# Performance work log

Hardware: AMD Instinct MI355X
Metric: run time of the kernel (lower is better)

## Reference

```python
import jax, jax.numpy as jnp
import numpy as np

B, Hd, Wd, C, NH, WS = 8, 128, 128, 192, 6, 8
HDIM = int(C * 2.0)   # FFN hidden = 384
RED = C // 8          # AIM channel-gate reduction = 24


def setup_inputs() -> dict:
    key = jax.random.key(0)
    ks = jax.random.split(key, 12)
    s = 0.02
    return {
        "x": jax.random.normal(ks[0], (B, Hd * Wd, C), jnp.float32),
        "H": Hd,
        "W": Wd,
        "n1_w": jnp.ones((C,), jnp.float32),
        "n1_b": jnp.zeros((C,), jnp.float32),
        "qkv_w": jax.random.normal(ks[1], (C, 3 * C), jnp.float32) * s,
        "proj_w": jax.random.normal(ks[2], (C, C), jnp.float32) * s,
        "proj_b": jnp.zeros((C,), jnp.float32),
        "attn_bias": jax.random.normal(ks[3], (NH, WS * WS, WS * WS), jnp.float32) * s,
        "conv_w": jax.random.normal(ks[4], (C, 1, 3, 3), jnp.float32) * s,
        "cg_w1": jax.random.normal(ks[5], (RED, C), jnp.float32) * s,
        "cg_w2": jax.random.normal(ks[6], (C, RED), jnp.float32) * s,
        "n2_w": jnp.ones((C,), jnp.float32),
        "n2_b": jnp.zeros((C,), jnp.float32),
        "fc1_w": jax.random.normal(ks[7], (C, HDIM), jnp.float32) * s,
        "smix_w": jax.random.normal(ks[8], (HDIM, 1, 3, 3), jnp.float32) * s,
        "fc2_w": jax.random.normal(ks[9], (HDIM, C), jnp.float32) * s,
    }


def _ln(x, w, b):
    m = x.mean(-1, keepdims=True)
    v = ((x - m) ** 2).mean(-1, keepdims=True)
    return (x - m) * jax.lax.rsqrt(v + 1e-5) * w + b


def _dwconv(x, w, H, W):
    # x: [B, L, Cx] -> depthwise 3x3 'same' conv -> [B, L, Cx]
    Bx, L, Cx = x.shape
    xi = x.transpose(0, 2, 1).reshape(Bx, Cx, H, W)
    y = jax.lax.conv_general_dilated(
        xi, w, (1, 1), 'SAME', feature_group_count=Cx,
        dimension_numbers=('NCHW', 'OIHW', 'NCHW'))
    return y.reshape(Bx, Cx, L).transpose(0, 2, 1)


def _window_attn(x, H, W, qkv_w, proj_w, proj_b, bias):
    Bx, L, Cx = x.shape
    nHw, nWw = H // WS, W // WS  # H, W are multiples of WS here (no padding needed)
    hd = Cx // NH
    # [B, L, C] -> [B*nH*nW, ws*ws, C]
    xw = (x.reshape(Bx, nHw, WS, nWw, WS, Cx)
           .transpose(0, 1, 3, 2, 4, 5)
           .reshape(Bx * nHw * nWw, WS * WS, Cx))
    qkv = (xw @ qkv_w).reshape(-1, WS * WS, 3, NH, hd).transpose(2, 0, 3, 1, 4)
    q, k, v = qkv[0], qkv[1], qkv[2]          # [Bw, nh, N, hd]
    logits = (q * hd ** -0.5) @ k.transpose(0, 1, 3, 2) + bias[None]
    attn = jax.nn.softmax(logits, axis=-1)
    out = (attn @ v).transpose(0, 2, 1, 3).reshape(-1, WS * WS, Cx)
    out = out @ proj_w + proj_b
    # windows -> [B, L, C]
    return (out.reshape(Bx, nHw, nWw, WS, WS, Cx)
               .transpose(0, 1, 3, 2, 4, 5)
               .reshape(Bx, L, Cx))


def reference(x, H, W, n1_w, n1_b, qkv_w, proj_w, proj_b, attn_bias,
              conv_w, cg_w1, cg_w2, n2_w, n2_b, fc1_w, smix_w, fc2_w):
    n1 = _ln(x, n1_w, n1_b)
    attn_feat = _window_attn(n1, H, W, qkv_w, proj_w, proj_b, attn_bias)
    conv_feat = jax.nn.gelu(_dwconv(n1, conv_w, H, W), approximate=False)
    # AIM: channel_modulates_spatial (btype == 'spatial')
    pooled = conv_feat.mean(axis=1)                                   # [B, C]
    cm = jax.nn.sigmoid(jax.nn.gelu(pooled @ cg_w1.T, approximate=False) @ cg_w2.T)
    x = x + attn_feat * cm[:, None, :] + conv_feat                    # residual (DropPath=id)
    # FFN with depthwise spatial mixing
    n2 = _ln(x, n2_w, n2_b)
    h = jax.nn.gelu(n2 @ fc1_w, approximate=False)                    # [B, L, HDIM]
    h = _dwconv(h, smix_w, H, W)
    return x + h @ fc2_w
```

## Files before the change

kernel.cpp:

```cpp
#include <hip/hip_runtime.h>
#include <hip/hip_bf16.h>
#include <math.h>

#define BATCH 8
#define CCH 192
#define LTOK 16384
#define BL 131072LL
#define NWIN 2048
#define NHEADS 6

typedef __hip_bfloat16 bf16;
typedef __bf16 bfr;
typedef bfr bf16x8 __attribute__((ext_vector_type(8)));
typedef float f32x4 __attribute__((ext_vector_type(4)));
typedef unsigned short u16x8 __attribute__((ext_vector_type(8)));
typedef unsigned short u16x4 __attribute__((ext_vector_type(4)));
typedef unsigned int u32x2 __attribute__((ext_vector_type(2)));

#define FX     0
#define FN1W   1
#define FN1B   2
#define FQKVW  3
#define FPROJW 4
#define FPROJB 5
#define FBIAS  6
#define FCONVW 7
#define FCG1   8
#define FCG2   9
#define FN2W   10
#define FN2B   11
#define FFC1   12
#define FSMIX  13
#define FFC2   14

struct InPtrs { const void* p[15]; int n[15]; };

__device__ __forceinline__ float ldin(const void* p, long long i, int f32) {
    return f32 ? ((const float*)p)[i]
               : __bfloat162float(((const bf16*)p)[i]);
}

__device__ __forceinline__ float bfcvt(unsigned short u) {
    return __uint_as_float((unsigned)u << 16);
}

__device__ __forceinline__ f32x4 ld4f(const void* p, long long i, int f32) {
    if (f32) return *(const f32x4*)((const float*)p + i);
    u16x4 v = *(const u16x4*)((const bf16*)p + i);
    f32x4 r;
    r[0] = bfcvt(v[0]); r[1] = bfcvt(v[1]); r[2] = bfcvt(v[2]); r[3] = bfcvt(v[3]);
    return r;
}
__device__ __forceinline__ f32x4 ld4b(const bf16* p, long long i) {
    u16x4 v = *(const u16x4*)(p + i);
    f32x4 r;
    r[0] = bfcvt(v[0]); r[1] = bfcvt(v[1]); r[2] = bfcvt(v[2]); r[3] = bfcvt(v[3]);
    return r;
}
__device__ __forceinline__ void st4b(bf16* p, long long i, f32x4 v) {
    union { bf16 h; unsigned short u; } cv;
    u16x4 o;
    cv.h = __float2bfloat16(v[0]); o[0] = cv.u;
    cv.h = __float2bfloat16(v[1]); o[1] = cv.u;
    cv.h = __float2bfloat16(v[2]); o[2] = cv.u;
    cv.h = __float2bfloat16(v[3]); o[3] = cv.u;
    *(u16x4*)(p + i) = o;
}

__device__ __forceinline__ unsigned pk2bf(float a, float b) {
    union { bf16 h; unsigned short u; } ca, cb;
    ca.h = __float2bfloat16(a);
    cb.h = __float2bfloat16(b);
    return (unsigned)ca.u | ((unsigned)cb.u << 16);
}

__device__ __forceinline__ float gelu_f(float v) {
    return 0.5f * v * (1.0f + erff(v * 0.70710678118654752f));
}

__device__ int local_probe(const void* p_, int n) {
    __shared__ int sh0, sh1, sh2;
    if (threadIdx.x == 0) { sh0 = 0; sh1 = 0; sh2 = 0; }
    __syncthreads();
    const bf16* p = (const bf16*)p_;
    int m = n < 2048 ? n : 2048;
    bool insane = false, evennz = false, oddnz = false;
    for (int i = threadIdx.x; i < m; i += 256) {
        float v = __bfloat162float(p[i]);
        if (!(fabsf(v) <= 1e9f)) insane = true;
        if (v != 0.0f) { if (i & 1) oddnz = true; else evennz = true; }
    }
    if (insane) sh0 = 1;
    if (evennz) sh1 = 1;
    if (oddnz)  sh2 = 1;
    __syncthreads();
    return (sh0 || (!sh1 && sh2)) ? 1 : 0;
}

__global__ __launch_bounds__(256)
void prep_k(InPtrs ip, int* __restrict__ flags,
            bf16* __restrict__ qkv_wT, bf16* __restrict__ proj_wT,
            bf16* __restrict__ fc1_wT, bf16* __restrict__ fc2_wT,
            float* __restrict__ convwT, float* __restrict__ smixwT,
            float* __restrict__ pooled) {
    int blk = blockIdx.x;
    if (blk < 15) {
        int f = local_probe(ip.p[blk], ip.n[blk]);
        if (threadIdx.x == 0) flags[blk] = f;
        return;
    }
    blk -= 15;
    if (blk < 432) {
        int f = local_probe(ip.p[FQKVW], ip.n[FQKVW]);
        int idx = blk * 256 + threadIdx.x;
        int k = idx / 576, n = idx - k * 576;
        qkv_wT[(long long)n * 192 + k] = __float2bfloat16(ldin(ip.p[FQKVW], idx, f));
        return;
    }
    blk -= 432;
    if (blk < 144) {
        int f = local_probe(ip.p[FPROJW], ip.n[FPROJW]);
        int idx = blk * 256 + threadIdx.x;
        int k = idx / 192, n = idx - k * 192;
        proj_wT[(long long)n * 192 + k] = __float2bfloat16(ldin(ip.p[FPROJW], idx, f));
        return;
    }
    blk -= 144;
    if (blk < 288) {
        int f = local_probe(ip.p[FFC1], ip.n[FFC1]);
        int idx = blk * 256 + threadIdx.x;
        int k = idx / 384, n = idx - k * 384;
        fc1_wT[(long long)n * 192 + k] = __float2bfloat16(ldin(ip.p[FFC1], idx, f));
        return;
    }
    blk -= 288;
    if (blk < 288) {
        int f = local_probe(ip.p[FFC2], ip.n[FFC2]);
        int idx = blk * 256 + threadIdx.x;
        int k = idx / 192, n = idx - k * 192;
        fc2_wT[(long long)n * 384 + k] = __float2bfloat16(ldin(ip.p[FFC2], idx, f));
        return;
    }
    blk -= 288;
    if (blk < 7) {
        int f = local_probe(ip.p[FCONVW], ip.n[FCONVW]);
        int idx = blk * 256 + threadIdx.x;
        if (idx < 192 * 9) {
            int c = idx / 9, t = idx - c * 9;
            convwT[t * 192 + c] = ldin(ip.p[FCONVW], idx, f);
        }
        return;
    }
    blk -= 7;
    if (blk < 14) {
        int f = local_probe(ip.p[FSMIX], ip.n[FSMIX]);
        int idx = blk * 256 + threadIdx.x;
        if (idx < 384 * 9) {
            int c = idx / 9, t = idx - c * 9;
            smixwT[t * 384 + c] = ldin(ip.p[FSMIX], idx, f);
        }
        return;
    }
    blk -= 14;
    {
        int idx = blk * 256 + threadIdx.x;
        if (idx < BATCH * CCH) pooled[idx] = 0.f;
    }
}

__global__ __launch_bounds__(256)
void ln_kernel(const void* __restrict__ x, const void* __restrict__ w,
               const void* __restrict__ b, bf16* __restrict__ out,
               const int* flags) {
    int fx = flags[FX], fw = flags[FN1W], fb = flags[FN1B];
    int wv = threadIdx.x >> 6, lane = threadIdx.x & 63;
    int gw = lane >> 4, l16 = lane & 15;
    long long t = (long long)blockIdx.x * 16 + wv * 4 + gw;
    long long base = t * CCH;
    f32x4 v[3];
#pragma unroll
    for (int k = 0; k < 3; ++k)
        v[k] = ld4f(x, base + l16 * 4 + 64 * k, fx);
    float s = 0.f;
#pragma unroll
    for (int k = 0; k < 3; ++k) s += v[k][0] + v[k][1] + v[k][2] + v[k][3];
    s += __shfl_xor(s, 1); s += __shfl_xor(s, 2);
    s += __shfl_xor(s, 4); s += __shfl_xor(s, 8);
    float mean = s * (1.0f / 192.0f);
    float vs = 0.f;
#pragma unroll
    for (int k = 0; k < 3; ++k)
#pragma unroll
        for (int j = 0; j < 4; ++j) {
            float d = v[k][j] - mean;
            vs += d * d;
        }
    vs += __shfl_xor(vs, 1); vs += __shfl_xor(vs, 2);
    vs += __shfl_xor(vs, 4); vs += __shfl_xor(vs, 8);
    float rstd = rsqrtf(vs * (1.0f / 192.0f) + 1e-5f);
#pragma unroll
    for (int k = 0; k < 3; ++k) {
        int c0 = l16 * 4 + 64 * k;
        f32x4 wv4 = ld4f(w, c0, fw);
        f32x4 bv4 = ld4f(b, c0, fb);
        f32x4 o;
#pragma unroll
        for (int j = 0; j < 4; ++j)
            o[j] = (v[k][j] - mean) * rstd * wv4[j] + bv4[j];
        st4b(out, base + c0, o);
    }
}

template<int EPI, int KK, int NN, typename CT>
__global__ __launch_bounds__(256)
void gemm2_k(const bf16* __restrict__ A_, const bf16* __restrict__ BT_,
             CT* __restrict__ Cmat, const void* __restrict__ bias,
             const float* __restrict__ res, const int* __restrict__ flags) {
    constexpr int KT = KK / 192;
    constexpr int NC = NN / 64;
    constexpr int NITER = NC * KT;
    constexpr int GSTR = KK * 2;
    constexpr bool WINM = (EPI == 0);
    __shared__ __align__(16) char Ts[64 * 384];

    const int fb = (EPI == 1) ? flags[FPROJB] : 0;
    const int tid = threadIdx.x;
    const int lane = tid & 63, wv = tid >> 6;
    const int r16 = lane & 15, q = lane >> 4;
    const long long m0 = (long long)blockIdx.x * 64;
    const int swz = (r16 & 7) << 4;

    const int wdx = blockIdx.x;
    const int wb = wdx >> 8, wrem = wdx & 255, wy = wrem >> 4, wx = wrem & 15;
    const long long tokbase = (long long)wb * LTOK + (wy * 8) * 128 + wx * 8;

    f32x4 pre[6];
    auto loadB = [&](int itn) {
        int nc2 = itn / KT, kt2 = itn - nc2 * KT;
#pragma unroll
        for (int p = 0; p < 6; ++p) {
            int off = p * 4096 + tid * 16;
            int row = off / 384, col = off - row * 384;
            pre[p] = *(const f32x4*)((const char*)BT_ +
                     (long long)(nc2 * 64 + row) * GSTR + kt2 * 384 + col);
        }
    };
    auto writeT = [&]() {
#pragma unroll
        for (int p = 0; p < 6; ++p) {
            int off = p * 4096 + tid * 16;
            int row = off / 384, col = off - row * 384;
            *(f32x4*)(Ts + row * 384 + (col ^ ((row & 7) << 4))) = pre[p];
        }
    };

    loadB(0);

    bf16x8 afrag[KK / 32];
    const char* Arow = Ts + (wv * 16 + r16) * 384;
    const char* asrc = (const char*)A_;
#pragma unroll
    for (int kt = 0; kt < KT; ++kt) {
#pragma unroll
        for (int p = 0; p < 6; ++p) {
            int off = p * 4096 + tid * 16;
            int row = off / 384, col = off - row * 384;
            long long grow = WINM ? (tokbase + (row >> 3) * 128 + (row & 7))
                                  : (m0 + row);
            *(f32x4*)(Ts + row * 384 + (col ^ ((row & 7) << 4))) =
                *(const f32x4*)(asrc + grow * GSTR + kt * 384 + col);
        }
        __syncthreads();
#pragma unroll
        for (int ks = 0; ks < 6; ++ks)
            afrag[kt * 6 + ks] = *(const bf16x8*)(Arow + ((ks * 64 + q * 16) ^ swz));
        __syncthreads();
    }
    writeT();
    __syncthreads();

    f32x4 acc0, acc1, acc2, acc3;
    float resv[16];

    for (int it = 0; it < NITER; ++it) {
        const int nc = it / KT, kt = it - nc * KT;
        if (kt == 0) {
            acc0 = f32x4{0.f, 0.f, 0.f, 0.f};
            acc1 = acc0; acc2 = acc0; acc3 = acc0;
            if (EPI == 3) {
#pragma unroll
                for (int j = 0; j < 4; ++j)
#pragma unroll
                    for (int r = 0; r < 4; ++r)
                        resv[j * 4 + r] =
                            res[(m0 + wv * 16 + q * 4 + r) * NN + nc * 64 + j * 16 + r16];
            }
        }
        const bool nxt = (it + 1 < NITER);
        if (nxt) loadB(it + 1);
#pragma unroll
        for (int ks = 0; ks < 6; ++ks) {
            bf16x8 a = afrag[kt * 6 + ks];
            const char* bb = Ts + r16 * 384 + ((ks * 64 + q * 16) ^ swz);
            bf16x8 b0 = *(const bf16x8*)(bb);
            bf16x8 b1 = *(const bf16x8*)(bb + 16 * 384);
            bf16x8 b2 = *(const bf16x8*)(bb + 32 * 384);
            bf16x8 b3 = *(const bf16x8*)(bb + 48 * 384);
            acc0 = __builtin_amdgcn_mfma_f32_16x16x32_bf16(a, b0, acc0, 0, 0, 0);
            acc1 = __builtin_amdgcn_mfma_f32_16x16x32_bf16(a, b1, acc1, 0, 0, 0);
            acc2 = __builtin_amdgcn_mfma_f32_16x16x32_bf16(a, b2, acc2, 0, 0, 0);
            acc3 = __builtin_amdgcn_mfma_f32_16x16x32_bf16(a, b3, acc3, 0, 0, 0);
        }
        __syncthreads();
        if (nxt) writeT();
        if (kt == KT - 1) {
            f32x4 accs[4] = {acc0, acc1, acc2, acc3};
#pragma unroll
            for (int j = 0; j < 4; ++j) {
                int col = nc * 64 + j * 16 + r16;
#pragma unroll
                for (int r = 0; r < 4; ++r) {
                    float v = accs[j][r];
                    if (EPI == 1) v += ldin(bias, col, fb);
                    if (EPI == 2) v = gelu_f(v);
                    if (EPI == 3) v += resv[j * 4 + r];
                    if (WINM) {
                        int tin = wv * 16 + q * 4 + r;
                        int sel = col / 192, rem2 = col - sel * 192;
                        int hh = rem2 >> 5, d = rem2 & 31;
                        Cmat[((((long long)sel * NWIN + wdx) * 6 + hh) * 64 + tin) * 32 + d] = (CT)v;
                    } else {
                        long long row = m0 + wv * 16 + q * 4 + r;
                        Cmat[row * NN + col] = (CT)v;
                    }
                }
            }
        }
        if (nxt) __syncthreads();
    }
}

__global__ __launch_bounds__(384)
void attn_proj_k(const bf16* __restrict__ qkvw, const void* __restrict__ bias,
                 const bf16* __restrict__ pwT, const void* __restrict__ proj_b,
                 bf16* __restrict__ attnf, const int* __restrict__ flags) {
    __shared__ __align__(16) char SM[24576];

    const int fbias = flags[FBIAS];
    const int h = threadIdx.x >> 6, lane = threadIdx.x & 63;
    const int w = blockIdx.x;
    const int l15 = lane & 15, quad = lane >> 4;
    bfr* vtp = (bfr*)(SM + h * 4096);

    const bfr* qb = (const bfr*)qkvw + ((long long)w * 6 + h) * 2048;
    const bfr* kb = qb + (long long)NWIN * 6 * 2048;
    const bfr* vb = kb + (long long)NWIN * 6 * 2048;

    const bfr* vp = vb + lane * 32;
    bf16x8 v0 = *(const bf16x8*)(vp);
    bf16x8 v1 = *(const bf16x8*)(vp + 8);
    bf16x8 v2 = *(const bf16x8*)(vp + 16);
    bf16x8 v3 = *(const bf16x8*)(vp + 24);

    bf16x8 aq[4], bk[4];
#pragma unroll
    for (int mt = 0; mt < 4; ++mt) {
        int off = (mt * 16 + l15) * 32 + quad * 8;
        aq[mt] = *(const bf16x8*)(qb + off);
        bk[mt] = *(const bf16x8*)(kb + off);
    }

#pragma unroll
    for (int j = 0; j < 8; ++j) {
        int sc = lane ^ (j << 3);
        vtp[j * 64 + sc]        = v0[j];
        vtp[(j + 8) * 64 + sc]  = v1[j];
        vtp[(j + 16) * 64 + sc] = v2[j];
        vtp[(j + 24) * 64 + sc] = v3[j];
    }

    f32x4 T[4][4];
#pragma unroll
    for (int ti = 0; ti < 4; ++ti)
#pragma unroll
        for (int tj = 0; tj < 4; ++tj) {
            f32x4 z = {0.f, 0.f, 0.f, 0.f};
            T[ti][tj] = __builtin_amdgcn_mfma_f32_16x16x32_bf16(bk[ti], aq[tj], z, 0, 0, 0);
        }

    const float scale = 0.17677669529663689f;
    const long long bias0 = (long long)h * 4096;
    unsigned Wreg[4][4][2];
#pragma unroll
    for (int tj = 0; tj < 4; ++tj) {
        const long long brow = bias0 + (tj * 16 + l15) * 64 + quad * 4;
        float mloc = -3.0e38f;
#pragma unroll
        for (int ti = 0; ti < 4; ++ti) {
            f32x4 bv4 = ld4f(bias, brow + ti * 16, fbias);
#pragma unroll
            for (int r = 0; r < 4; ++r) {
                float v = T[ti][tj][r] * scale + bv4[r];
                T[ti][tj][r] = v;
                mloc = fmaxf(mloc, v);
            }
        }
        mloc = fmaxf(mloc, __shfl_xor(mloc, 16));
        mloc = fmaxf(mloc, __shfl_xor(mloc, 32));
        float l = 0.f;
#pragma unroll
        for (int ti = 0; ti < 4; ++ti)
#pragma unroll
            for (int r = 0; r < 4; ++r) {
                float e = __expf(T[ti][tj][r] - mloc);
                T[ti][tj][r] = e;
                l += e;
            }
        l += __shfl_xor(l, 16);
        l += __shfl_xor(l, 32);
        float linv = 1.0f / l;
#pragma unroll
        for (int ti = 0; ti < 4; ++ti) {
            Wreg[tj][ti][0] = pk2bf(T[ti][tj][0] * linv, T[ti][tj][1] * linv);
            Wreg[tj][ti][1] = pk2bf(T[ti][tj][2] * linv, T[ti][tj][3] * linv);
        }
    }

    const int vsw = (l15 & 7) << 3;
    bf16x8 bv[2][2];
#pragma unroll
    for (int kc = 0; kc < 2; ++kc) {
        bv[kc][0] = *(const bf16x8*)&vtp[l15 * 64 + ((kc * 32 + quad * 8) ^ vsw)];
        bv[kc][1] = *(const bf16x8*)&vtp[(16 + l15) * 64 + ((kc * 32 + quad * 8) ^ vsw)];
    }
    const int hi = quad >> 1, qlow = quad & 1;
    f32x4 O[4][2];
#pragma unroll
    for (int tj = 0; tj < 4; ++tj) {
        O[tj][0] = f32x4{0.f, 0.f, 0.f, 0.f};
        O[tj][1] = O[tj][0];
    }
#pragma unroll
    for (int tj = 0; tj < 4; ++tj)
#pragma unroll
        for (int kc = 0; kc < 2; ++kc) {
            union { unsigned u[4]; bf16x8 v; } ap;
#pragma unroll
            for (int j2 = 0; j2 < 4; ++j2) {
                int srcl = (2 * qlow + (j2 >> 1)) * 16 + l15;
                unsigned va = (unsigned)__shfl((int)Wreg[tj][2 * kc][j2 & 1], srcl);
                unsigned vb2 = (unsigned)__shfl((int)Wreg[tj][2 * kc + 1][j2 & 1], srcl);
                ap.u[j2] = hi ? vb2 : va;
            }
            O[tj][0] = __builtin_amdgcn_mfma_f32_16x16x32_bf16(ap.v, bv[kc][0], O[tj][0], 0, 0, 0);
            O[tj][1] = __builtin_amdgcn_mfma_f32_16x16x32_bf16(ap.v, bv[kc][1], O[tj][1], 0, 0, 0);
        }

    const int fpb = flags[FPROJB];
    bf16x8 pw[2][6];
    float pbv[2];
#pragma unroll
    for (int nt = 0; nt < 2; ++nt) {
        int col = h * 32 + nt * 16 + l15;
        pbv[nt] = ldin(proj_b, col, fpb);
#pragma unroll
        for (int ks = 0; ks < 6; ++ks)
            pw[nt][ks] = *(const bf16x8*)((const bfr*)pwT + (long long)col * 192 + ks * 32 + quad * 8);
    }

    __syncthreads();

#pragma unroll
    for (int tj = 0; tj < 4; ++tj)
#pragma unroll
        for (int n2 = 0; n2 < 2; ++n2)
#pragma unroll
            for (int r = 0; r < 4; ++r) {
                int row = tj * 16 + quad * 4 + r;
                int cb = (h * 64 + n2 * 32 + l15 * 2) ^ ((row & 7) << 4);
                *(bf16*)(SM + row * 384 + cb) = __float2bfloat16(O[tj][n2][r]);
            }

    __syncthreads();

    const int csw = (l15 & 7) << 4;
    f32x4 pacc[4][2];
#pragma unroll
    for (int mt = 0; mt < 4; ++mt) {
        pacc[mt][0] = f32x4{0.f, 0.f, 0.f, 0.f};
        pacc[mt][1] = pacc[mt][0];
    }
#pragma unroll
    for (int ks = 0; ks < 6; ++ks) {
        bf16x8 af[4];
#pragma unroll
        for (int mt = 0; mt < 4; ++mt)
            af[mt] = *(const bf16x8*)(SM + (mt * 16 + l15) * 384 +
                                      ((ks * 64 + quad * 16) ^ csw));
#pragma unroll
        for (int nt = 0; nt < 2; ++nt)
#pragma unroll
            for (int mt = 0; mt < 4; ++mt)
                pacc[mt][nt] = __builtin_amdgcn_mfma_f32_16x16x32_bf16(af[mt], pw[nt][ks], pacc[mt][nt], 0, 0, 0);
    }

#pragma unroll
    for (int nt = 0; nt < 2; ++nt) {
        int col = h * 32 + nt * 16 + l15;
#pragma unroll
        for (int mt = 0; mt < 4; ++mt)
#pragma unroll
            for (int r = 0; r < 4; ++r) {
                long long row = (long long)w * 64 + mt * 16 + quad * 4 + r;
                attnf[row * CCH + col] = __float2bfloat16(pacc[mt][nt][r] + pbv[nt]);
            }
    }
}

template<bool GELU, int CX>
__global__ __launch_bounds__(256)
void dwconv_s4_k(const bf16* __restrict__ in, const float* __restrict__ wt,
                 bf16* __restrict__ out) {
    constexpr int CG = CX / 8;
    int cpx = gridDim.x >> 3;
    int lb = (blockIdx.x & 7) * cpx + (blockIdx.x >> 3);
    long long idx = (long long)lb * 256 + threadIdx.x;
    if (idx >= (BL / 4) * CG) return;
    int cg = (int)(idx % CG);
    long long s = idx / CG;
    int xs = (int)(s & 31);
    long long by = s >> 5;
    int y = (int)(by & 127);
    int x0 = xs * 4;
    int c0 = cg * 8;
    const long long rowpix = by * 128;

    float acc[4][8] = {};
#pragma unroll
    for (int dy = -1; dy <= 1; ++dy) {
        int yy = y + dy;
        if (yy < 0 || yy > 127) continue;
        const bf16* rp = in + ((rowpix + dy * 128) + x0) * CX + c0;
        float fcol[6][8];
#pragma unroll
        for (int ci = 0; ci < 6; ++ci) {
            int xx = x0 + ci - 1;
            if (xx < 0 || xx > 127) {
#pragma unroll
                for (int j = 0; j < 8; ++j) fcol[ci][j] = 0.f;
            } else {
                u16x8 v = *(const u16x8*)(rp + (ci - 1) * CX);
#pragma unroll
                for (int j = 0; j < 8; ++j) fcol[ci][j] = bfcvt(v[j]);
            }
        }
        const float* wb = wt + (dy + 1) * 3 * CX + c0;
#pragma unroll
        for (int dx = 0; dx < 3; ++dx) {
            f32x4 w0 = *(const f32x4*)(wb + dx * CX);
            f32x4 w1 = *(const f32x4*)(wb + dx * CX + 4);
#pragma unroll
            for (int px = 0; px < 4; ++px) {
#pragma unroll
                for (int j = 0; j < 4; ++j) {
                    acc[px][j]     += fcol[px + dx][j]     * w0[j];
                    acc[px][j + 4] += fcol[px + dx][j + 4] * w1[j];
                }
            }
        }
    }
#pragma unroll
    for (int px = 0; px < 4; ++px) {
        __attribute__((aligned(16))) unsigned short ob[8];
#pragma unroll
        for (int j = 0; j < 8; ++j) {
            float vv = acc[px][j];
            if (GELU) vv = gelu_f(vv);
            union { bf16 h; unsigned short u; } cv;
            cv.h = __float2bfloat16(vv);
            ob[j] = cv.u;
        }
        *(u16x8*)(out + (rowpix + x0 + px) * CX + c0) = *(const u16x8*)ob;
    }
}

__global__ __launch_bounds__(192)
void pool_k(const bf16* __restrict__ conv, float* __restrict__ pooled) {
    __shared__ float red[8][192];
    int b = blockIdx.x, chunk = blockIdx.y;
    int cg = threadIdx.x % 24, rr = threadIdx.x / 24;
    float acc[8] = {0.f, 0.f, 0.f, 0.f, 0.f, 0.f, 0.f, 0.f};
    long long rowbase = (long long)b * LTOK + chunk * 256;
    for (int r = rr; r < 256; r += 8) {
        u16x8 v = *(const u16x8*)(conv + (rowbase + r) * CCH + cg * 8);
#pragma unroll
        for (int j = 0; j < 8; ++j) acc[j] += bfcvt(v[j]);
    }
#pragma unroll
    for (int j = 0; j < 8; ++j) red[rr][cg * 8 + j] = acc[j];
    __syncthreads();
    if (rr == 0) {
#pragma unroll
        for (int j = 0; j < 8; ++j) {
            float s = 0.f;
#pragma unroll
            for (int i = 0; i < 8; ++i) s += red[i][cg * 8 + j];
            atomicAdd(&pooled[b * CCH + cg * 8 + j], s);
        }
    }
}

__global__ void cm_k(const float* __restrict__ pooled, const void* __restrict__ w1,
                     const void* __restrict__ w2, float* __restrict__ cm,
                     const int* flags) {
    __shared__ float ps[192], g[24];
    int f1 = flags[FCG1], f2 = flags[FCG2];
    int b = blockIdx.x, c = threadIdx.x;
    ps[c] = pooled[b * CCH + c] * (1.0f / 16384.0f);
    __syncthreads();
    if (c < 24) {
        float t = 0.f;
        for (int k = 0; k < 192; ++k) t += ps[k] * ldin(w1, c * 192 + k, f1);
        g[c] = gelu_f(t);
    }
    __syncthreads();
    float s = 0.f;
#pragma unroll
    for (int r = 0; r < 24; ++r) s += g[r] * ldin(w2, c * 24 + r, f2);
    cm[b * CCH + c] = 1.0f / (1.0f + expf(-s));
}

__global__ __launch_bounds__(256)
void x2ln2_k(const void* __restrict__ x, const bf16* __restrict__ attnf,
             const bf16* __restrict__ conv, const float* __restrict__ cm,
             const void* __restrict__ w, const void* __restrict__ bb,
             float* __restrict__ x2, bf16* __restrict__ n2, const int* flags) {
    int fx = flags[FX], fw = flags[FN2W], fb = flags[FN2B];
    int wv = threadIdx.x >> 6, lane = threadIdx.x & 63;
    int gw = lane >> 4, l16 = lane & 15;
    long long t = (long long)blockIdx.x * 16 + wv * 4 + gw;
    int b = (int)(t >> 14);
    int l = (int)(t & 16383);
    int y = l >> 7, xx = l & 127;
    long long wrow = ((long long)b * 256 + (y >> 3) * 16 + (xx >> 3)) * 64 + (y & 7) * 8 + (xx & 7);

    f32x4 sv[3];
#pragma unroll
    for (int k = 0; k < 3; ++k) {
        int c0 = l16 * 4 + 64 * k;
        f32x4 xv  = ld4f(x, t * CCH + c0, fx);
        f32x4 af  = ld4b(attnf, wrow * CCH + c0);
        f32x4 cf  = ld4b(conv, t * CCH + c0);
        f32x4 cmv = *(const f32x4*)(cm + b * CCH + c0);
        f32x4 o;
#pragma unroll
        for (int j = 0; j < 4; ++j)
            o[j] = xv[j] + af[j] * cmv[j] + cf[j];
        *(f32x4*)(x2 + t * CCH + c0) = o;
        sv[k] = o;
    }
    float s = 0.f;
#pragma unroll
    for (int k = 0; k < 3; ++k) s += sv[k][0] + sv[k][1] + sv[k][2] + sv[k][3];
    s += __shfl_xor(s, 1); s += __shfl_xor(s, 2);
    s += __shfl_xor(s, 4); s += __shfl_xor(s, 8);
    float mean = s * (1.0f / 192.0f);
    float vs = 0.f;
#pragma unroll
    for (int k = 0; k < 3; ++k)
#pragma unroll
        for (int j = 0; j < 4; ++j) {
            float d = sv[k][j] - mean;
            vs += d * d;
        }
    vs += __shfl_xor(vs, 1); vs += __shfl_xor(vs, 2);
    vs += __shfl_xor(vs, 4); vs += __shfl_xor(vs, 8);
    float rstd = rsqrtf(vs * (1.0f / 192.0f) + 1e-5f);
#pragma unroll
    for (int k = 0; k < 3; ++k) {
        int c0 = l16 * 4 + 64 * k;
        f32x4 wv4 = ld4f(w, c0, fw);
        f32x4 bv4 = ld4f(bb, c0, fb);
        f32x4 o;
#pragma unroll
        for (int j = 0; j < 4; ++j)
            o[j] = (sv[k][j] - mean) * rstd * wv4[j] + bv4[j];
        st4b(n2, t * CCH + c0, o);
    }
}

extern "C" void kernel_launch(void* const* d_in, const int* in_sizes, int n_in,
                              void* d_out, int out_size, void* d_ws, size_t ws_size,
                              hipStream_t stream) {
    (void)n_in; (void)out_size; (void)ws_size;
    float* out = (float*)d_out;

    char* wsp = (char*)d_ws;
    size_t off = 0;
    auto alloc = [&](size_t bytes) -> char* {
        char* p = wsp + off;
        off += (bytes + 255) & ~(size_t)255;
        return p;
    };
    int*  flags   = (int*)alloc(15 * 4);
    bf16* qkv_wT  = (bf16*)alloc(576 * 192 * 2);
    bf16* proj_wT = (bf16*)alloc(192 * 192 * 2);
    bf16* fc1_wT  = (bf16*)alloc(384 * 192 * 2);
    bf16* fc2_wT  = (bf16*)alloc(192 * 384 * 2);
    float* convwT = (float*)alloc(9 * CCH * 4);
    float* smixwT = (float*)alloc(9 * 384 * 4);
    float* pooled = (float*)alloc(BATCH * CCH * 4);
    float* cm     = (float*)alloc(BATCH * CCH * 4);
    char* Rbig    = alloc(BL * 576 * 2);
    char* Rpair   = alloc(BL * 384 * 2);

    bf16* qkvb  = (bf16*)Rbig;
    bf16* convf = (bf16*)Rbig;
    bf16* hbuf  = (bf16*)Rbig;
    bf16* n1    = (bf16*)Rpair;
    bf16* attnf = (bf16*)(Rpair + (size_t)BL * 192 * 2);
    bf16* n2    = n1;
    bf16* h2    = (bf16*)Rpair;
    float* x2   = out;

    const int imap[15] = {0, 3, 4, 5, 6, 7, 8, 9, 10, 11, 12, 13, 14, 15, 16};
    InPtrs ip;
    for (int i = 0; i < 15; ++i) { ip.p[i] = d_in[imap[i]]; ip.n[i] = in_sizes[imap[i]]; }
    const void* x        = d_in[0];
    const void* proj_b   = d_in[7];
    const void* attnbias = d_in[8];
    const void* cg_w1    = d_in[10];
    const void* cg_w2    = d_in[11];

    prep_k<<<1194, 256, 0, stream>>>(ip, flags, qkv_wT, proj_wT, fc1_wT, fc2_wT,
                                     convwT, smixwT, pooled);

    ln_kernel<<<BL / 16, 256, 0, stream>>>(x, d_in[3], d_in[4], n1, flags);
    gemm2_k<0, 192, 576, bf16><<<BL / 64, 256, 0, stream>>>(n1, qkv_wT, qkvb, nullptr, nullptr, flags);
    attn_proj_k<<<NWIN, 384, 0, stream>>>(qkvb, attnbias, proj_wT, proj_b, attnf, flags);
    dwconv_s4_k<true, 192><<<(int)(BL / 4 * 24 / 256), 256, 0, stream>>>(n1, convwT, convf);
    pool_k<<<dim3(BATCH, 64), 192, 0, stream>>>(convf, pooled);
    cm_k<<<BATCH, 192, 0, stream>>>(pooled, cg_w1, cg_w2, cm, flags);
    x2ln2_k<<<BL / 16, 256, 0, stream>>>(x, attnf, convf, cm, d_in[12], d_in[13], x2, n2, flags);
    gemm2_k<2, 192, 384, bf16><<<BL / 64, 256, 0, stream>>>(n2, fc1_wT, hbuf, nullptr, nullptr, flags);
    dwconv_s4_k<false, 384><<<(int)(BL / 4 * 48 / 256), 256, 0, stream>>>(hbuf, smixwT, h2);
    gemm2_k<3, 384, 192, float><<<BL / 64, 256, 0, stream>>>(h2, fc2_wT, out, nullptr, x2, flags);
}
```

Before: 599.1 us.

## Split window attention across two waves per head to double parallelism

The window-attention kernel now launches 768 threads per window, so each head gets two waves that each handle half of the query row-tiles. Only the first wave of each head stages V into shared memory, and an extra barrier is added before V is read. The projection is split so each wave computes one 16-column slice. This lowers per-wave register pressure and latency, at the cost of duplicated K loads and more barriers per block.

After: 591.3 us. About the same (-1.3%).

```diff
diff --git a/kernel.cpp b/kernel.cpp
--- a/kernel.cpp
+++ b/kernel.cpp
@@ -340,14 +340,15 @@
     }
 }
 
-__global__ __launch_bounds__(384)
+__global__ __launch_bounds__(768)
 void attn_proj_k(const bf16* __restrict__ qkvw, const void* __restrict__ bias,
                  const bf16* __restrict__ pwT, const void* __restrict__ proj_b,
                  bf16* __restrict__ attnf, const int* __restrict__ flags) {
     __shared__ __align__(16) char SM[24576];
 
     const int fbias = flags[FBIAS];
-    const int h = threadIdx.x >> 6, lane = threadIdx.x & 63;
+    const int wid = threadIdx.x >> 6, lane = threadIdx.x & 63;
+    const int h = wid >> 1, half = wid & 1;
     const int w = blockIdx.x;
     const int l15 = lane & 15, quad = lane >> 4;
     bfr* vtp = (bfr*)(SM + h * 4096);
@@ -356,43 +357,42 @@
     const bfr* kb = qb + (long long)NWIN * 6 * 2048;
     const bfr* vb = kb + (long long)NWIN * 6 * 2048;
 
-    const bfr* vp = vb + lane * 32;
-    bf16x8 v0 = *(const bf16x8*)(vp);
-    bf16x8 v1 = *(const bf16x8*)(vp + 8);
-    bf16x8 v2 = *(const bf16x8*)(vp + 16);
-    bf16x8 v3 = *(const bf16x8*)(vp + 24);
-
-    bf16x8 aq[4], bk[4];
-#pragma unroll
-    for (int mt = 0; mt < 4; ++mt) {
-        int off = (mt * 16 + l15) * 32 + quad * 8;
-        aq[mt] = *(const bf16x8*)(qb + off);
-        bk[mt] = *(const bf16x8*)(kb + off);
-    }
-
-#pragma unroll
-    for (int j = 0; j < 8; ++j) {
-        int sc = lane ^ (j << 3);
-        vtp[j * 64 + sc]        = v0[j];
-        vtp[(j + 8) * 64 + sc]  = v1[j];
-        vtp[(j + 16) * 64 + sc] = v2[j];
-        vtp[(j + 24) * 64 + sc] = v3[j];
-    }
-
-    f32x4 T[4][4];
+    if (half == 0) {
+        const bfr* vp = vb + lane * 32;
+        bf16x8 v0 = *(const bf16x8*)(vp);
+        bf16x8 v1 = *(const bf16x8*)(vp + 8);
+        bf16x8 v2 = *(const bf16x8*)(vp + 16);
+        bf16x8 v3 = *(const bf16x8*)(vp + 24);
+#pragma unroll
+        for (int j = 0; j < 8; ++j) {
+            int sc = lane ^ (j << 3);
+            vtp[j * 64 + sc]        = v0[j];
+            vtp[(j + 8) * 64 + sc]  = v1[j];
+            vtp[(j + 16) * 64 + sc] = v2[j];
+            vtp[(j + 24) * 64 + sc] = v3[j];
+        }
+    }
+
+    bf16x8 bk[4], aq[2];
 #pragma unroll
     for (int ti = 0; ti < 4; ++ti)
-#pragma unroll
-        for (int tj = 0; tj < 4; ++tj) {
-            f32x4 z = {0.f, 0.f, 0.f, 0.f};
-            T[ti][tj] = __builtin_amdgcn_mfma_f32_16x16x32_bf16(bk[ti], aq[tj], z, 0, 0, 0);
-        }
+        bk[ti] = *(const bf16x8*)(kb + (ti * 16 + l15) * 32 + quad * 8);
+#pragma unroll
+    for (int tj2 = 0; tj2 < 2; ++tj2)
+        aq[tj2] = *(const bf16x8*)(qb + ((half * 2 + tj2) * 16 + l15) * 32 + quad * 8);
 
     const float scale = 0.17677669529663689f;
     const long long bias0 = (long long)h * 4096;
-    unsigned Wreg[4][4][2];
-#pragma unroll
-    for (int tj = 0; tj < 4; ++tj) {
+    unsigned Wreg[2][4][2];
+#pragma unroll
+    for (int tj2 = 0; tj2 < 2; ++tj2) {
+        const int tj = half * 2 + tj2;
+        f32x4 T[4];
+#pragma unroll
+        for (int ti = 0; ti < 4; ++ti) {
+            f32x4 z = {0.f, 0.f, 0.f, 0.f};
+            T[ti] = __builtin_amdgcn_mfma_f32_16x16x32_bf16(bk[ti], aq[tj2], z, 0, 0, 0);
+        }
         const long long brow = bias0 + (tj * 16 + l15) * 64 + quad * 4;
         float mloc = -3.0e38f;
 #pragma unroll
@@ -400,8 +400,8 @@
             f32x4 bv4 = ld4f(bias, brow + ti * 16, fbias);
 #pragma unroll
             for (int r = 0; r < 4; ++r) {
-                float v = T[ti][tj][r] * scale + bv4[r];
-                T[ti][tj][r] = v;
+                float v = T[ti][r] * scale + bv4[r];
+                T[ti][r] = v;
                 mloc = fmaxf(mloc, v);
             }
         }
@@ -412,8 +412,8 @@
         for (int ti = 0; ti < 4; ++ti)
 #pragma unroll
             for (int r = 0; r < 4; ++r) {
-                float e = __expf(T[ti][tj][r] - mloc);
-                T[ti][tj][r] = e;
+                float e = __expf(T[ti][r] - mloc);
+                T[ti][r] = e;
                 l += e;
             }
         l += __shfl_xor(l, 16);
@@ -421,10 +421,12 @@
         float linv = 1.0f / l;
 #pragma unroll
         for (int ti = 0; ti < 4; ++ti) {
-            Wreg[tj][ti][0] = pk2bf(T[ti][tj][0] * linv, T[ti][tj][1] * linv);
-            Wreg[tj][ti][1] = pk2bf(T[ti][tj][2] * linv, T[ti][tj][3] * linv);
-        }
-    }
+            Wreg[tj2][ti][0] = pk2bf(T[ti][0] * linv, T[ti][1] * linv);
+            Wreg[tj2][ti][1] = pk2bf(T[ti][2] * linv, T[ti][3] * linv);
+        }
+    }
+
+    __syncthreads();
 
     const int vsw = (l15 & 7) << 3;
     bf16x8 bv[2][2];
@@ -434,87 +436,73 @@
         bv[kc][1] = *(const bf16x8*)&vtp[(16 + l15) * 64 + ((kc * 32 + quad * 8) ^ vsw)];
     }
     const int hi = quad >> 1, qlow = quad & 1;
-    f32x4 O[4][2];
-#pragma unroll
-    for (int tj = 0; tj < 4; ++tj) {
-        O[tj][0] = f32x4{0.f, 0.f, 0.f, 0.f};
-        O[tj][1] = O[tj][0];
-    }
-#pragma unroll
-    for (int tj = 0; tj < 4; ++tj)
+    f32x4 O[2][2];
+#pragma unroll
+    for (int tj2 = 0; tj2 < 2; ++tj2) {
+        O[tj2][0] = f32x4{0.f, 0.f, 0.f, 0.f};
+        O[tj2][1] = O[tj2][0];
+    }
+#pragma unroll
+    for (int tj2 = 0; tj2 < 2; ++tj2)
 #pragma unroll
         for (int kc = 0; kc < 2; ++kc) {
             union { unsigned u[4]; bf16x8 v; } ap;
 #pragma unroll
             for (int j2 = 0; j2 < 4; ++j2) {
                 int srcl = (2 * qlow + (j2 >> 1)) * 16 + l15;
-                unsigned va = (unsigned)__shfl((int)Wreg[tj][2 * kc][j2 & 1], srcl);
-                unsigned vb2 = (unsigned)__shfl((int)Wreg[tj][2 * kc + 1][j2 & 1], srcl);
+                unsigned va = (unsigned)__shfl((int)Wreg[tj2][2 * kc][j2 & 1], srcl);
+                unsigned vb2 = (unsigned)__shfl((int)Wreg[tj2][2 * kc + 1][j2 & 1], srcl);
                 ap.u[j2] = hi ? vb2 : va;
             }
-            O[tj][0] = __builtin_amdgcn_mfma_f32_16x16x32_bf16(ap.v, bv[kc][0], O[tj][0], 0, 0, 0);
-            O[tj][1] = __builtin_amdgcn_mfma_f32_16x16x32_bf16(ap.v, bv[kc][1], O[tj][1], 0, 0, 0);
+            O[tj2][0] = __builtin_amdgcn_mfma_f32_16x16x32_bf16(ap.v, bv[kc][0], O[tj2][0], 0, 0, 0);
+            O[tj2][1] = __builtin_amdgcn_mfma_f32_16x16x32_bf16(ap.v, bv[kc][1], O[tj2][1], 0, 0, 0);
         }
 
     const int fpb = flags[FPROJB];
-    bf16x8 pw[2][6];
-    float pbv[2];
-#pragma unroll
-    for (int nt = 0; nt < 2; ++nt) {
-        int col = h * 32 + nt * 16 + l15;
-        pbv[nt] = ldin(proj_b, col, fpb);
-#pragma unroll
-        for (int ks = 0; ks < 6; ++ks)
-            pw[nt][ks] = *(const bf16x8*)((const bfr*)pwT + (long long)col * 192 + ks * 32 + quad * 8);
-    }
-
-    __syncthreads();
-
-#pragma unroll
-    for (int tj = 0; tj < 4; ++tj)
+    const int pcol = wid * 16 + l15;
+    float pbv = ldin(proj_b, pcol, fpb);
+    bf16x8 pw[6];
+#pragma unroll
+    for (int ks = 0; ks < 6; ++ks)
+        pw[ks] = *(const bf16x8*)((const bfr*)pwT + (long long)pcol * 192 + ks * 32 + quad * 8);
+
+    __syncthreads();
+
+#pragma unroll
+    for (int tj2 = 0; tj2 < 2; ++tj2)
 #pragma unroll
         for (int n2 = 0; n2 < 2; ++n2)
 #pragma unroll
             for (int r = 0; r < 4; ++r) {
-                int row = tj * 16 + quad * 4 + r;
+                int row = (half * 2 + tj2) * 16 + quad * 4 + r;
                 int cb = (h * 64 + n2 * 32 + l15 * 2) ^ ((row & 7) << 4);
-                *(bf16*)(SM + row * 384 + cb) = __float2bfloat16(O[tj][n2][r]);
+                *(bf16*)(SM + row * 384 + cb) = __float2bfloat16(O[tj2][n2][r]);
             }
 
     __syncthreads();
 
     const int csw = (l15 & 7) << 4;
-    f32x4 pacc[4][2];
-#pragma unroll
-    for (int mt = 0; mt < 4; ++mt) {
-        pacc[mt][0] = f32x4{0.f, 0.f, 0.f, 0.f};
-        pacc[mt][1] = pacc[mt][0];
-    }
+    f32x4 pacc[4];
+#pragma unroll
+    for (int mt = 0; mt < 4; ++mt)
+        pacc[mt] = f32x4{0.f, 0.f, 0.f, 0.f};
 #pragma unroll
     for (int ks = 0; ks < 6; ++ks) {
-        bf16x8 af[4];
-#pragma unroll
-        for (int mt = 0; mt < 4; ++mt)
-            af[mt] = *(const bf16x8*)(SM + (mt * 16 + l15) * 384 +
-                                      ((ks * 64 + quad * 16) ^ csw));
-#pragma unroll
-        for (int nt = 0; nt < 2; ++nt)
-#pragma unroll
-            for (int mt = 0; mt < 4; ++mt)
-                pacc[mt][nt] = __builtin_amdgcn_mfma_f32_16x16x32_bf16(af[mt], pw[nt][ks], pacc[mt][nt], 0, 0, 0);
-    }
-
-#pragma unroll
-    for (int nt = 0; nt < 2; ++nt) {
-        int col = h * 32 + nt * 16 + l15;
-#pragma unroll
-        for (int mt = 0; mt < 4; ++mt)
-#pragma unroll
-            for (int r = 0; r < 4; ++r) {
-                long long row = (long long)w * 64 + mt * 16 + quad * 4 + r;
-                attnf[row * CCH + col] = __float2bfloat16(pacc[mt][nt][r] + pbv[nt]);
-            }
-    }
+#pragma unroll
+        for (int mt = 0; mt < 4; ++mt) {
+            bf16x8 af = *(const bf16x8*)(SM + (mt * 16 + l15) * 384 +
+                                         ((ks * 64 + quad * 16) ^ csw));
+            pacc[mt] = __builtin_amdgcn_mfma_f32_16x16x32_bf16(af, pw[ks], pacc[mt], 0, 0, 0);
+        }
+    }
+
+#pragma unroll
+    for (int mt = 0; mt < 4; ++mt)
+#pragma unroll
+        for (int r = 0; r < 4; ++r) {
+            long long row = (long long)w * 64 + mt * 16 + quad * 4 + r;
+            attnf[row * CCH + pcol] = __float2bfloat16(pacc[mt][r] + pbv);
+        }
 }
 
 template<bool GELU, int CX>
@@ -737,7 +725,7 @@
 
     ln_kernel<<<BL / 16, 256, 0, stream>>>(x, d_in[3], d_in[4], n1, flags);
     gemm2_k<0, 192, 576, bf16><<<BL / 64, 256, 0, stream>>>(n1, qkv_wT, qkvb, nullptr, nullptr, flags);
-    attn_proj_k<<<NWIN, 384, 0, stream>>>(qkvb, attnbias, proj_wT, proj_b, attnf, flags);
+    attn_proj_k<<<NWIN, 768, 0, stream>>>(qkvb, attnbias, proj_wT, proj_b, attnf, flags);
     dwconv_s4_k<true, 192><<<(int)(BL / 4 * 24 / 256), 256, 0, stream>>>(n1, convwT, convf);
     pool_k<<<dim3(BATCH, 64), 192, 0, stream>>>(convf, pooled);
     cm_k<<<BATCH, 192, 0, stream>>>(pooled, cg_w1, cg_w2, cm, flags);
```
